# Performance work log

Hardware: AMD Instinct MI355X
Metric: run time of the kernel (lower is better)

## Reference

```python
import jax, jax.numpy as jnp
import numpy as np

N_NODES = 100000
N_EDGES = 1600000
D_IN = 128
HID = 64
N_LAYERS = 5
D_OUT = 32
N_GRAPHS = 1000


def setup_inputs() -> dict:
    key = jax.random.key(0)
    ks = jax.random.split(key, 12)
    node_embed = jax.random.normal(ks[0], (N_NODES, D_IN), dtype=jnp.float32)
    edge_index = jax.random.randint(ks[1], (2, N_EDGES), 0, N_NODES, dtype=jnp.int32)
    batch = jnp.sort(jax.random.randint(ks[2], (N_NODES,), 0, N_GRAPHS, dtype=jnp.int32))
    s = 0.1  # weight scale
    return {
        "node_embed": node_embed,
        "edge_index": edge_index,
        "batch": batch,
        "W_in": s * jax.random.normal(ks[3], (D_IN, HID), dtype=jnp.float32),
        "b_in": s * jax.random.normal(ks[4], (HID,), dtype=jnp.float32),
        "ggnn_w": s * jax.random.normal(ks[5], (N_LAYERS, HID, HID), dtype=jnp.float32),
        "gru_w_ih": s * jax.random.normal(ks[6], (3 * HID, HID), dtype=jnp.float32),
        "gru_w_hh": s * jax.random.normal(ks[7], (3 * HID, HID), dtype=jnp.float32),
        "gru_b_ih": s * jax.random.normal(ks[8], (3 * HID,), dtype=jnp.float32),
        "gru_b_hh": s * jax.random.normal(ks[9], (3 * HID,), dtype=jnp.float32),
        "W_out": s * jax.random.normal(ks[10], (HID, D_OUT), dtype=jnp.float32),
        "b_out": s * jax.random.normal(ks[11], (D_OUT,), dtype=jnp.float32),
    }


def _gru_cell(m, h, w_ih, w_hh, b_ih, b_hh):
    # torch.nn.GRUCell: gates ordered (r, z, n)
    gi = m @ w_ih.T + b_ih   # [N, 3H]
    gh = h @ w_hh.T + b_hh   # [N, 3H]
    i_r, i_z, i_n = jnp.split(gi, 3, axis=-1)
    h_r, h_z, h_n = jnp.split(gh, 3, axis=-1)
    r = jax.nn.sigmoid(i_r + h_r)
    z = jax.nn.sigmoid(i_z + h_z)
    n = jnp.tanh(i_n + r * h_n)
    return (1.0 - z) * n + z * h


def reference(node_embed, edge_index, batch, W_in, b_in, ggnn_w,
              gru_w_ih, gru_w_hh, gru_b_ih, gru_b_hh, W_out, b_out):
    n_nodes = node_embed.shape[0]
    src, dst = edge_index[0], edge_index[1]

    # input linear: [N, D_IN] -> [N, H]
    x = node_embed @ W_in + b_in

    # GatedGraphConv: per-layer linear message, add-aggregate, shared GRU update
    def layer(h, w):
        m = h @ w                                   # [N, H]
        agg = jax.ops.segment_sum(m[src], dst, num_segments=n_nodes)  # scatter-add
        h_new = _gru_cell(agg, h, gru_w_ih, gru_w_hh, gru_b_ih, gru_b_hh)
        return h_new, None

    x, _ = jax.lax.scan(layer, x, ggnn_w)

    # global mean pool over graphs
    sums = jax.ops.segment_sum(x, batch, num_segments=N_GRAPHS)       # [G, H]
    cnts = jax.ops.segment_sum(jnp.ones((n_nodes,), x.dtype), batch, num_segments=N_GRAPHS)
    pooled = sums / jnp.maximum(cnts, 1.0)[:, None]

    # dropout is identity in eval mode
    return pooled @ W_out + b_out
```

## Files before the change

kernel.cpp:

```cpp
#include <hip/hip_runtime.h>

#define N_NODES 100000
#define N_EDGES 1600000
#define D_IN 128
#define HID 64
#define N_LAYERS 5
#define D_OUT 32
#define N_GRAPHS 1000

#define LNB 32
#define LR 8

#define BSHIFT 7
#define NBUCK ((N_NODES + 127) >> BSHIFT)
#define CNT_B 256
#define EPB (N_EDGES / CNT_B)
#define NT (NBUCK * CNT_B)

typedef unsigned short ushort_t;
typedef unsigned int uint_t;
typedef __attribute__((ext_vector_type(8))) short short8;
typedef __attribute__((ext_vector_type(4))) float f32x4;

#define MFMA(a, b, c) __builtin_amdgcn_mfma_f32_16x16x32_bf16((a), (b), (c), 0, 0, 0)

#define WSTRIDE (24 * 2 * 64 * 8)

#define INPUT_B (N_NODES / LNB)
#define PREP_B  ((N_LAYERS * WSTRIDE + 255) / 256)

__device__ __forceinline__ float fast_sigmoid(float x) {
    return __builtin_amdgcn_rcpf(1.0f + __expf(-x));
}
__device__ __forceinline__ float fast_tanh(float x) {
    return 1.0f - 2.0f * __builtin_amdgcn_rcpf(1.0f + __expf(2.0f * x));
}
__device__ __forceinline__ ushort_t f2bf(float f) {
    uint_t u = __float_as_uint(f);
    return (ushort_t)((u + 0x7fffu + ((u >> 16) & 1u)) >> 16);
}
__device__ __forceinline__ float b2f(ushort_t u) {
    return __uint_as_float(((uint_t)u) << 16);
}

__global__ __launch_bounds__(256) void k_count(const int* __restrict__ ei,
                                               int* __restrict__ table) {
    __shared__ int hcnt[NBUCK];
    int b = blockIdx.x, tid = threadIdx.x;
    for (int i = tid; i < NBUCK; i += 256) hcnt[i] = 0;
    __syncthreads();
    int e0 = b * EPB;
    for (int i = tid; i < EPB; i += 256)
        atomicAdd(&hcnt[ei[N_EDGES + e0 + i] >> BSHIFT], 1);
    __syncthreads();
    for (int i = tid; i < NBUCK; i += 256)
        table[i * CNT_B + b] = hcnt[i];
}

#define SCHUNK 1024
__global__ __launch_bounds__(1024) void k_tscan1(int* __restrict__ table,
                                                 int* __restrict__ bsum) {
    __shared__ int buf[SCHUNK];
    int tid = threadIdx.x;
    int i = blockIdx.x * SCHUNK + tid;
    int v = (i < NT) ? table[i] : 0;
    buf[tid] = v;
    __syncthreads();
    for (int s = 1; s < SCHUNK; s <<= 1) {
        int a = (tid >= s) ? buf[tid - s] : 0;
        __syncthreads();
        buf[tid] += a;
        __syncthreads();
    }
    if (i < NT) table[i] = buf[tid] - v;
    if (tid == SCHUNK - 1) bsum[blockIdx.x] = buf[tid];
}

__global__ void k_tscan2(int* __restrict__ bsum, int nchunks,
                         float* __restrict__ sums) {
    int b = blockIdx.x;
    if (b == 0) {
        if (threadIdx.x == 0) {
            int carry = 0;
            for (int c = 0; c < nchunks; ++c) {
                int t = bsum[c];
                bsum[c] = carry;
                carry += t;
            }
        }
        return;
    }
    int i = (b - 1) * 256 + threadIdx.x;
    if (i < N_GRAPHS * (HID + 1)) sums[i] = 0.0f;
}

__global__ void k_tscan3(int* __restrict__ table, const int* __restrict__ bsum) {
    int i = blockIdx.x * blockDim.x + threadIdx.x;
    if (i < NT) table[i] += bsum[i >> 10];
}

__global__ __launch_bounds__(256) void k_scatin(
        const int* __restrict__ ei, const int* __restrict__ table,
        uint2* __restrict__ eb,
        const float* __restrict__ ggnn_w, const float* __restrict__ w_ih,
        const float* __restrict__ w_hh,
        short* __restrict__ Whi, short* __restrict__ Wlo,
        const float* __restrict__ ne, const float* __restrict__ W_in,
        const float* __restrict__ b_in,
        ushort_t* __restrict__ hbhi, ushort_t* __restrict__ hblo) {
    __shared__ int cur[NBUCK];
    __shared__ float sE[LNB][D_IN];
    int b = blockIdx.x;
    int tid = threadIdx.x;

    if (b < CNT_B) {
        for (int i = tid; i < NBUCK; i += 256) cur[i] = table[i * CNT_B + b];
        __syncthreads();
        int e0 = b * EPB;
        for (int i = tid; i < EPB; i += 256) {
            int s = ei[e0 + i];
            int d = ei[N_EDGES + e0 + i];
            int pos = atomicAdd(&cur[d >> BSHIFT], 1);
            uint2 v; v.x = (uint_t)s; v.y = (uint_t)d;
            eb[pos] = v;
        }
        return;
    }
    if (b < CNT_B + PREP_B) {
        int t = (b - CNT_B) * 256 + tid;
        if (t >= N_LAYERS * WSTRIDE) return;
        int i    = t & 7;
        int lane = (t >> 3) & 63;
        int s    = (t >> 9) & 1;
        int tt   = (t >> 10) % 24;
        int lay  = (t >> 10) / 24;
        int k    = s * 32 + (lane >> 4) * 8 + i;
        int col  = tt * 16 + (lane & 15);
        float val;
        if (col < 192) {
            const float* wl = ggnn_w + ((size_t)lay * HID + k) * HID;
            const float* wi = w_ih + (size_t)col * HID;
            float acc = 0.0f;
#pragma unroll 8
            for (int q = 0; q < HID; ++q) acc = fmaf(wl[q], wi[q], acc);
            val = acc;
        } else {
            val = w_hh[(size_t)(col - 192) * HID + k];
        }
        ushort_t h_ = f2bf(val);
        Whi[t] = (short)h_;
        Wlo[t] = (short)f2bf(val - b2f(h_));
        return;
    }
    int j = tid & 63, w = tid >> 6;
    int nodeBase = (b - CNT_B - PREP_B) * LNB;
    {
        const float4* g = (const float4*)(ne + (size_t)nodeBase * D_IN);
        float4* l = (float4*)&sE[0][0];
        for (int i = tid; i < LNB * D_IN / 4; i += 256) l[i] = g[i];
    }
    __syncthreads();
    float acc[LR];
#pragma unroll
    for (int r = 0; r < LR; ++r) acc[r] = 0.0f;
#pragma unroll 4
    for (int k = 0; k < D_IN; ++k) {
        float wv = W_in[k * HID + j];
#pragma unroll
        for (int r = 0; r < LR; ++r)
            acc[r] = fmaf(sE[w * LR + r][k], wv, acc[r]);
    }
    float bb = b_in[j];
#pragma unroll
    for (int r = 0; r < LR; ++r) {
        int n = nodeBase + w * LR + r;
        float v = acc[r] + bb;
        ushort_t hi = f2bf(v);
        size_t idx = (size_t)n * HID + j;
        hbhi[idx] = hi;
        hblo[idx] = f2bf(v - b2f(hi));
    }
}

__global__ __launch_bounds__(256) void k_csr(const int* __restrict__ table,
                                             const uint2* __restrict__ eb,
                                             int* __restrict__ csr,
                                             int* __restrict__ off) {
    __shared__ int cnt[128];
    __shared__ int slot[128];
    int b = blockIdx.x, tid = threadIdx.x;
    int nodeBase = b << BSHIFT;
    int nn = min(128, N_NODES - nodeBase);
    int beg = table[b * CNT_B];
    int end = (b == NBUCK - 1) ? N_EDGES : table[(b + 1) * CNT_B];

    if (tid < 128) { cnt[tid] = 0; slot[tid] = 0; }
    __syncthreads();
    for (int i = beg + tid; i < end; i += 256)
        atomicAdd(&cnt[eb[i].y & 127], 1);
    __syncthreads();

    int orig = (tid < 128) ? cnt[tid] : 0;
    for (int s = 1; s < 128; s <<= 1) {
        int a = (tid >= s && tid < 128) ? cnt[tid - s] : 0;
        __syncthreads();
        if (tid < 128) cnt[tid] += a;
        __syncthreads();
    }
    int start = 0;
    if (tid < 128) start = beg + cnt[tid] - orig;
    __syncthreads();
    if (tid < 128) {
        cnt[tid] = start;
        if (tid < nn) off[nodeBase + tid] = start;
    }
    if (b == NBUCK - 1 && tid == 0) off[N_NODES] = N_EDGES;
    __syncthreads();

    for (int i = beg + tid; i < end; i += 256) {
        uint2 e = eb[i];
        int ln = e.y & 127;
        int p = cnt[ln] + atomicAdd(&slot[ln], 1);
        csr[p] = (int)e.x;
    }
}

__global__ __launch_bounds__(256) void k_gather(const int* __restrict__ off,
                                                const int* __restrict__ csr,
                                                const ushort_t* __restrict__ hb,
                                                ushort_t* __restrict__ aggb) {
    int t = blockIdx.x * blockDim.x + threadIdx.x;
    int n = t >> 6;
    int lane = t & 63;
    int q = lane >> 3, c = lane & 7;
    int beg = off[n], end = off[n + 1];
    float a[8];
#pragma unroll
    for (int x = 0; x < 8; ++x) a[x] = 0.f;
#pragma unroll 2
    for (int i = beg; i < end; i += 8) {
        int idx = i + q;
        int sidx = csr[min(idx, end - 1)];
        float msk = (idx < end) ? 1.0f : 0.0f;
        uint4 v = *(const uint4*)(hb + (size_t)sidx * HID + c * 8);
        a[0] = fmaf(msk, __uint_as_float(v.x << 16), a[0]);
        a[1] = fmaf(msk, __uint_as_float(v.x & 0xffff0000u), a[1]);
        a[2] = fmaf(msk, __uint_as_float(v.y << 16), a[2]);
        a[3] = fmaf(msk, __uint_as_float(v.y & 0xffff0000u), a[3]);
        a[4] = fmaf(msk, __uint_as_float(v.z << 16), a[4]);
        a[5] = fmaf(msk, __uint_as_float(v.z & 0xffff0000u), a[5]);
        a[6] = fmaf(msk, __uint_as_float(v.w << 16), a[6]);
        a[7] = fmaf(msk, __uint_as_float(v.w & 0xffff0000u), a[7]);
    }
#pragma unroll
    for (int x = 0; x < 8; ++x) {
        a[x] += __shfl_xor(a[x], 8);
        a[x] += __shfl_xor(a[x], 16);
        a[x] += __shfl_xor(a[x], 32);
    }
    if (q == 0) {
        uint4 o;
        o.x = (uint_t)f2bf(a[0]) | ((uint_t)f2bf(a[1]) << 16);
        o.y = (uint_t)f2bf(a[2]) | ((uint_t)f2bf(a[3]) << 16);
        o.z = (uint_t)f2bf(a[4]) | ((uint_t)f2bf(a[5]) << 16);
        o.w = (uint_t)f2bf(a[6]) | ((uint_t)f2bf(a[7]) << 16);
        *(uint4*)(aggb + (size_t)n * HID + c * 8) = o;
    }
}

__global__ __launch_bounds__(256) void k_gru(const ushort_t* __restrict__ aggb,
                                             ushort_t* __restrict__ hbhi,
                                             ushort_t* __restrict__ hblo,
                                             const short* __restrict__ Whi,
                                             const short* __restrict__ Wlo,
                                             const float* __restrict__ b_ih,
                                             const float* __restrict__ b_hh) {
    __shared__ short8 sW[24 * 2 * 64];
    int tid = threadIdx.x;
    {
        const short8* gW = (const short8*)Whi;
#pragma unroll
        for (int i = 0; i < 12; ++i) sW[tid + i * 256] = gW[tid + i * 256];
    }
    int wv = tid >> 6, l = tid & 63;
    int q = l >> 4, c = l & 15;
    int nodeBase = blockIdx.x * 64 + wv * 16;

    int anode = nodeBase + c;
    int acl = (anode < N_NODES) ? anode : (N_NODES - 1);
    const ushort_t* arow = aggb + (size_t)acl * HID;
    const ushort_t* hrowh = hbhi + (size_t)acl * HID;
    const ushort_t* hrowl = hblo + (size_t)acl * HID;
    short8 Ag[2], Ah_hi[2], Ah_lo[2];
    Ag[0] = *(const short8*)(arow + q * 8);
    Ag[1] = *(const short8*)(arow + 32 + q * 8);
    Ah_hi[0] = *(const short8*)(hrowh + q * 8);
    Ah_hi[1] = *(const short8*)(hrowh + 32 + q * 8);
    Ah_lo[0] = *(const short8*)(hrowl + q * 8);
    Ah_lo[1] = *(const short8*)(hrowl + 32 + q * 8);
    __syncthreads();

    f32x4 acc[24];
    const f32x4 zero = {0.f, 0.f, 0.f, 0.f};
#pragma unroll
    for (int t = 0; t < 24; ++t) acc[t] = zero;

    const short8* BH = sW + l;
    const short8* BL = ((const short8*)Wlo) + l;
#pragma unroll
    for (int t = 0; t < 24; ++t) {
        short8 b0h = BH[(t * 2 + 0) * 64];
        short8 b1h = BH[(t * 2 + 1) * 64];
        short8 b0l = BL[(t * 2 + 0) * 64];
        short8 b1l = BL[(t * 2 + 1) * 64];
        if (t < 12) {
            acc[t] = MFMA(Ag[0], b0h, acc[t]);
            acc[t] = MFMA(Ag[0], b0l, acc[t]);
            acc[t] = MFMA(Ag[1], b1h, acc[t]);
            acc[t] = MFMA(Ag[1], b1l, acc[t]);
        } else {
            acc[t] = MFMA(Ah_hi[0], b0h, acc[t]);
            acc[t] = MFMA(Ah_lo[0], b0h, acc[t]);
            acc[t] = MFMA(Ah_hi[0], b0l, acc[t]);
            acc[t] = MFMA(Ah_hi[1], b1h, acc[t]);
            acc[t] = MFMA(Ah_lo[1], b1h, acc[t]);
            acc[t] = MFMA(Ah_hi[1], b1l, acc[t]);
        }
    }

#pragma unroll
    for (int jb = 0; jb < 4; ++jb) {
        int j = jb * 16 + c;
        float br  = b_ih[j] + b_hh[j];
        float bz  = b_ih[64 + j] + b_hh[64 + j];
        float bin = b_ih[128 + j];
        float bhn = b_hh[128 + j];
#pragma unroll
        for (int i = 0; i < 4; ++i) {
            int m = nodeBase + q * 4 + i;
            if (m < N_NODES) {
                float ir = acc[jb][i],      iz = acc[4 + jb][i],  inn = acc[8 + jb][i];
                float hr = acc[12 + jb][i], hz = acc[16 + jb][i], hn = acc[20 + jb][i];
                float rr = fast_sigmoid(ir + hr + br);
                float zz = fast_sigmoid(iz + hz + bz);
                float nv = fast_tanh((inn + bin) + rr * (hn + bhn));
                size_t idx = (size_t)m * HID + j;
                float hold = b2f(hbhi[idx]) + b2f(hblo[idx]);
                float v = (1.0f - zz) * nv + zz * hold;
                ushort_t hi = f2bf(v);
                hbhi[idx] = hi;
                hblo[idx] = f2bf(v - b2f(hi));
            }
        }
    }
}

#define POOL_NPW 32
__global__ void k_pool(const ushort_t* __restrict__ hb,
                       const int* __restrict__ batch,
                       float* __restrict__ sums,
                       float* __restrict__ cntf) {
    int wid = (blockIdx.x * blockDim.x + threadIdx.x) >> 6;
    int j = threadIdx.x & 63;
    int base = wid * POOL_NPW;
    if (base >= N_NODES) return;
    int end = base + POOL_NPW;
    if (end > N_NODES) end = N_NODES;
    float acc = 0.f, c = 0.f;
    int curg = batch[base];
    for (int n = base; n < end; ++n) {
        int g = batch[n];
        if (g != curg) {
            atomicAdd(&sums[(size_t)curg * HID + j], acc);
            if (j == 0) atomicAdd(&cntf[curg], c);
            acc = 0.f; c = 0.f; curg = g;
        }
        acc += b2f(hb[(size_t)n * HID + j]);
        c += 1.f;
    }
    atomicAdd(&sums[(size_t)curg * HID + j], acc);
    if (j == 0) atomicAdd(&cntf[curg], c);
}

__global__ void k_out(const float* __restrict__ sums,
                      const float* __restrict__ cntf,
                      const float* __restrict__ W_out,
                      const float* __restrict__ b_out,
                      float* __restrict__ out) {
    int t = blockIdx.x * blockDim.x + threadIdx.x;
    if (t >= N_GRAPHS * D_OUT) return;
    int g = t / D_OUT, o = t % D_OUT;
    float inv_c = __builtin_amdgcn_rcpf(fmaxf(cntf[g], 1.0f));
    float acc = 0.0f;
#pragma unroll
    for (int k = 0; k < HID; ++k)
        acc = fmaf(sums[g * HID + k], W_out[k * D_OUT + o], acc);
    out[t] = acc * inv_c + b_out[o];
}

static inline char* align256(char* p) {
    return (char*)(((uintptr_t)p + 255) & ~(uintptr_t)255);
}

extern "C" void kernel_launch(void* const* d_in, const int* in_sizes, int n_in,
                              void* d_out, int out_size, void* d_ws, size_t ws_size,
                              hipStream_t stream) {
    const float* node_embed = (const float*)d_in[0];
    const int*   edge_index = (const int*)  d_in[1];
    const int*   batch      = (const int*)  d_in[2];
    const float* W_in       = (const float*)d_in[3];
    const float* b_in       = (const float*)d_in[4];
    const float* ggnn_w     = (const float*)d_in[5];
    const float* gru_w_ih   = (const float*)d_in[6];
    const float* gru_w_hh   = (const float*)d_in[7];
    const float* gru_b_ih   = (const float*)d_in[8];
    const float* gru_b_hh   = (const float*)d_in[9];
    const float* W_out      = (const float*)d_in[10];
    const float* b_out      = (const float*)d_in[11];
    float* out = (float*)d_out;

    char* p = (char*)d_ws;
    ushort_t* hbhi  = (ushort_t*)p; p = align256(p + (size_t)N_NODES * HID * sizeof(ushort_t));
    ushort_t* hblo  = (ushort_t*)p; p = align256(p + (size_t)N_NODES * HID * sizeof(ushort_t));
    ushort_t* aggb  = (ushort_t*)p; p = align256(p + (size_t)N_NODES * HID * sizeof(ushort_t));
    int*      csr   = (int*)p;      p = align256(p + (size_t)N_EDGES * sizeof(int));
    uint2*    eb    = (uint2*)p;    p = align256(p + (size_t)N_EDGES * sizeof(uint2));
    int*      table = (int*)p;      p = align256(p + (size_t)NT * sizeof(int));
    int*      off   = (int*)p;      p = align256(p + (size_t)(N_NODES + 1) * sizeof(int));
    int*      bsumT = (int*)p;      p = align256(p + 256 * sizeof(int));
    short*    Whi   = (short*)p;    p = align256(p + (size_t)N_LAYERS * WSTRIDE * sizeof(short));
    short*    Wlo   = (short*)p;    p = align256(p + (size_t)N_LAYERS * WSTRIDE * sizeof(short));
    float*    sums  = (float*)p;
    float*    cntf  = (float*)(p + (size_t)N_GRAPHS * HID * sizeof(float));

    const int BLK = 256;
    const int nchunksT = (NT + SCHUNK - 1) / SCHUNK;

    k_count<<<CNT_B, BLK, 0, stream>>>(edge_index, table);
    k_tscan1<<<nchunksT, SCHUNK, 0, stream>>>(table, bsumT);
    k_tscan2<<<1 + (N_GRAPHS * (HID + 1) + BLK - 1) / BLK, BLK, 0, stream>>>(
        bsumT, nchunksT, sums);
    k_tscan3<<<(NT + BLK - 1) / BLK, BLK, 0, stream>>>(table, bsumT);
    k_scatin<<<CNT_B + PREP_B + INPUT_B, BLK, 0, stream>>>(
        edge_index, table, eb,
        ggnn_w, gru_w_ih, gru_w_hh, Whi, Wlo,
        node_embed, W_in, b_in, hbhi, hblo);
    k_csr<<<NBUCK, BLK, 0, stream>>>(table, eb, csr, off);

    for (int l = 0; l < N_LAYERS; ++l) {
        k_gather<<<N_NODES * 64 / BLK, BLK, 0, stream>>>(off, csr, hbhi, aggb);
        k_gru<<<(N_NODES + 63) / 64, BLK, 0, stream>>>(
            aggb, hbhi, hblo, Whi + (size_t)l * WSTRIDE, Wlo + (size_t)l * WSTRIDE,
            gru_b_ih, gru_b_hh);
    }

    {
        int waves = (N_NODES + POOL_NPW - 1) / POOL_NPW;
        int threads = waves * 64;
        k_pool<<<(threads + BLK - 1) / BLK, BLK, 0, stream>>>(hbhi, batch, sums, cntf);
    }
    k_out<<<(N_GRAPHS * D_OUT + BLK - 1) / BLK, BLK, 0, stream>>>(sums, cntf, W_out, b_out, out);
}
```

Before: 483.3 us.

## Stage bucketed edge scatter in LDS and fold scan fixup into consumers

The edge scatter now does a block-local histogram and prefix scan, sorts its edges by bucket in shared memory, and then writes each bucket's edges to global memory as a contiguous run instead of random atomics to global positions. The separate k_tscan3 pass that added chunk offsets to the table is removed, and consumers add bsum on the fly. The weight-prep and input-linear work is split into its own kernel. Each scatter block now needs EPB*8 bytes (50 KB) of LDS plus its own recount of the destinations, which limits occupancy and adds a second read of the destination indices.

After: 499.1 us. 1.03x slower.

```diff
diff --git a/kernel.cpp b/kernel.cpp
--- a/kernel.cpp
+++ b/kernel.cpp
@@ -94,40 +94,73 @@
     if (i < N_GRAPHS * (HID + 1)) sums[i] = 0.0f;
 }
 
-__global__ void k_tscan3(int* __restrict__ table, const int* __restrict__ bsum) {
-    int i = blockIdx.x * blockDim.x + threadIdx.x;
-    if (i < NT) table[i] += bsum[i >> 10];
-}
-
-__global__ __launch_bounds__(256) void k_scatin(
-        const int* __restrict__ ei, const int* __restrict__ table,
-        uint2* __restrict__ eb,
+__global__ __launch_bounds__(256) void k_scatter(const int* __restrict__ ei,
+                                                 const int* __restrict__ table,
+                                                 const int* __restrict__ bsum,
+                                                 uint2* __restrict__ eb) {
+    __shared__ uint2 stage[EPB];
+    __shared__ int hoff[NBUCK];
+    __shared__ int hslot[NBUCK];
+    __shared__ int sbuf[256];
+    int b = blockIdx.x, tid = threadIdx.x;
+    for (int i = tid; i < NBUCK; i += 256) { hoff[i] = 0; hslot[i] = 0; }
+    __syncthreads();
+    int e0 = b * EPB;
+    for (int i = tid; i < EPB; i += 256)
+        atomicAdd(&hoff[ei[N_EDGES + e0 + i] >> BSHIFT], 1);
+    __syncthreads();
+    int base = tid * 4;
+    int c0 = (base + 0 < NBUCK) ? hoff[base + 0] : 0;
+    int c1 = (base + 1 < NBUCK) ? hoff[base + 1] : 0;
+    int c2 = (base + 2 < NBUCK) ? hoff[base + 2] : 0;
+    int c3 = (base + 3 < NBUCK) ? hoff[base + 3] : 0;
+    int tot = c0 + c1 + c2 + c3;
+    sbuf[tid] = tot;
+    __syncthreads();
+    for (int s = 1; s < 256; s <<= 1) {
+        int a = (tid >= s) ? sbuf[tid - s] : 0;
+        __syncthreads();
+        sbuf[tid] += a;
+        __syncthreads();
+    }
+    int mybase = sbuf[tid] - tot;
+    __syncthreads();
+    if (base + 0 < NBUCK) hoff[base + 0] = mybase;
+    if (base + 1 < NBUCK) hoff[base + 1] = mybase + c0;
+    if (base + 2 < NBUCK) hoff[base + 2] = mybase + c0 + c1;
+    if (base + 3 < NBUCK) hoff[base + 3] = mybase + c0 + c1 + c2;
+    __syncthreads();
+    for (int i = tid; i < EPB; i += 256) {
+        int s = ei[e0 + i];
+        int d = ei[N_EDGES + e0 + i];
+        int bk = d >> BSHIFT;
+        int pos = hoff[bk] + atomicAdd(&hslot[bk], 1);
+        uint2 v; v.x = (uint_t)s; v.y = (uint_t)d;
+        stage[pos] = v;
+    }
+    __syncthreads();
+    for (int p = tid; p < EPB; p += 256) {
+        uint2 e = stage[p];
+        int bk = (int)e.y >> BSHIFT;
+        int gidx = bk * CNT_B + b;
+        int gbase = table[gidx] + bsum[gidx >> 10];
+        eb[gbase + (p - hoff[bk])] = e;
+    }
+}
+
+__global__ __launch_bounds__(256) void k_prepin(
         const float* __restrict__ ggnn_w, const float* __restrict__ w_ih,
         const float* __restrict__ w_hh,
         short* __restrict__ Whi, short* __restrict__ Wlo,
         const float* __restrict__ ne, const float* __restrict__ W_in,
         const float* __restrict__ b_in,
         ushort_t* __restrict__ hbhi, ushort_t* __restrict__ hblo) {
-    __shared__ int cur[NBUCK];
     __shared__ float sE[LNB][D_IN];
     int b = blockIdx.x;
     int tid = threadIdx.x;
 
-    if (b < CNT_B) {
-        for (int i = tid; i < NBUCK; i += 256) cur[i] = table[i * CNT_B + b];
-        __syncthreads();
-        int e0 = b * EPB;
-        for (int i = tid; i < EPB; i += 256) {
-            int s = ei[e0 + i];
-            int d = ei[N_EDGES + e0 + i];
-            int pos = atomicAdd(&cur[d >> BSHIFT], 1);
-            uint2 v; v.x = (uint_t)s; v.y = (uint_t)d;
-            eb[pos] = v;
-        }
-        return;
-    }
-    if (b < CNT_B + PREP_B) {
-        int t = (b - CNT_B) * 256 + tid;
+    if (b < PREP_B) {
+        int t = b * 256 + tid;
         if (t >= N_LAYERS * WSTRIDE) return;
         int i    = t & 7;
         int lane = (t >> 3) & 63;
@@ -153,7 +186,7 @@
         return;
     }
     int j = tid & 63, w = tid >> 6;
-    int nodeBase = (b - CNT_B - PREP_B) * LNB;
+    int nodeBase = (b - PREP_B) * LNB;
     {
         const float4* g = (const float4*)(ne + (size_t)nodeBase * D_IN);
         float4* l = (float4*)&sE[0][0];
@@ -183,6 +216,7 @@
 }
 
 __global__ __launch_bounds__(256) void k_csr(const int* __restrict__ table,
+                                             const int* __restrict__ bsum,
                                              const uint2* __restrict__ eb,
                                              int* __restrict__ csr,
                                              int* __restrict__ off) {
@@ -191,8 +225,14 @@
     int b = blockIdx.x, tid = threadIdx.x;
     int nodeBase = b << BSHIFT;
     int nn = min(128, N_NODES - nodeBase);
-    int beg = table[b * CNT_B];
-    int end = (b == NBUCK - 1) ? N_EDGES : table[(b + 1) * CNT_B];
+    int i0 = b * CNT_B;
+    int beg = table[i0] + bsum[i0 >> 10];
+    int end;
+    if (b == NBUCK - 1) end = N_EDGES;
+    else {
+        int i1 = (b + 1) * CNT_B;
+        end = table[i1] + bsum[i1 >> 10];
+    }
 
     if (tid < 128) { cnt[tid] = 0; slot[tid] = 0; }
     __syncthreads();
@@ -440,12 +480,11 @@
     k_tscan1<<<nchunksT, SCHUNK, 0, stream>>>(table, bsumT);
     k_tscan2<<<1 + (N_GRAPHS * (HID + 1) + BLK - 1) / BLK, BLK, 0, stream>>>(
         bsumT, nchunksT, sums);
-    k_tscan3<<<(NT + BLK - 1) / BLK, BLK, 0, stream>>>(table, bsumT);
-    k_scatin<<<CNT_B + PREP_B + INPUT_B, BLK, 0, stream>>>(
-        edge_index, table, eb,
+    k_scatter<<<CNT_B, BLK, 0, stream>>>(edge_index, table, bsumT, eb);
+    k_prepin<<<PREP_B + INPUT_B, BLK, 0, stream>>>(
         ggnn_w, gru_w_ih, gru_w_hh, Whi, Wlo,
         node_embed, W_in, b_in, hbhi, hblo);
-    k_csr<<<NBUCK, BLK, 0, stream>>>(table, eb, csr, off);
+    k_csr<<<NBUCK, BLK, 0, stream>>>(table, bsumT, eb, csr, off);
 
     for (int l = 0; l < N_LAYERS; ++l) {
         k_gather<<<N_NODES * 64 / BLK, BLK, 0, stream>>>(off, csr, hbhi, aggb);
```
